# Optimization experiments

Measured on AMD Instinct MI355X. Metric: run time of the kernel, lower is better.

Reference implementation:

```python
import jax, jax.numpy as jnp
import numpy as np

EPS_NORM = 1e-12  # F.normalize eps
EPS_LOG = 1e-10
COMMITMENT_COST = 0.25


def setup_inputs() -> dict:
    key = jax.random.key(0)
    k1, k2 = jax.random.split(key)
    x = jax.random.normal(k1, (32, 256, 32, 32), dtype=jnp.float32)
    # nn.Embedding weight init: uniform(-1, 1)
    W = jax.random.uniform(k2, (1024, 256), dtype=jnp.float32, minval=-1.0, maxval=1.0)
    return {"x": x, "W": W, "n": 2}


def reference(x, W, n):
    sg = jax.lax.stop_gradient
    # NCHW -> NHWC
    inputs = jnp.transpose(x, (0, 2, 3, 1))
    B, H, Wd, D = inputs.shape
    K = W.shape[0]
    flat = inputs.reshape(-1, D)                       # [N, D]
    N = flat.shape[0]
    # squared euclidean distances via matmul: [N, K]
    distances = (jnp.sum(flat * flat, axis=1, keepdims=True)
                 + jnp.sum(W * W, axis=1)
                 - 2.0 * jnp.matmul(flat, W.T))
    # topk of -distances -> n smallest distances
    neg_vals, encoding_indices = jax.lax.top_k(-distances, n)  # [N, n]
    inv_dist = 1.0 / (-neg_vals)                        # 1/distance, [N, n]
    norm = jnp.maximum(jnp.sqrt(jnp.sum(inv_dist * inv_dist, axis=-1, keepdims=True)), EPS_NORM)
    weights = sg(inv_dist / norm)                       # detached in torch
    # scatter weights into one-hot-ish encodings [N, K]
    rows = jnp.arange(N)[:, None]
    encodings = jnp.zeros((N, K), dtype=flat.dtype).at[rows, encoding_indices].set(weights)
    quantized = jnp.matmul(encodings, W).reshape(B, H, Wd, D)
    e_latent_loss = jnp.mean((sg(quantized) - inputs) ** 2)
    q_latent_loss = jnp.mean((quantized - sg(inputs)) ** 2)
    loss = q_latent_loss + COMMITMENT_COST * e_latent_loss
    # straight-through
    quantized_st = inputs + sg(quantized - inputs)
    avg_probs = jnp.mean(encodings, axis=0)
    perplexity = jnp.exp(-jnp.sum(avg_probs * jnp.log(avg_probs + EPS_LOG)))
    return loss, jnp.transpose(quantized_st, (0, 3, 1, 2)), perplexity, encodings
```

## Files before the change

kernel.cpp:

```cpp
#include <hip/hip_runtime.h>
#include <math.h>

#define NROWS 32768
#define DIMS  256
#define KCODES 1024

typedef __attribute__((ext_vector_type(8))) short short8;
typedef __attribute__((ext_vector_type(4))) float f32x4;

static const size_t OFF_WB     = 8388608;
static const size_t OFF_WNORM  = OFF_WB + 131072;
static const size_t OFF_ENCSUM = OFF_WNORM + 1024;
static const size_t OFF_LOSSP  = OFF_ENCSUM + 1024;
static const size_t OFF_WND    = OFF_LOSSP + 8192;

static const size_t OUT_Q    = 1;
static const size_t OUT_PERP = 8388609;
static const size_t OUT_ENC  = 8388610;

__device__ inline unsigned short f2bf(float f) {
    unsigned int u = __float_as_uint(f);
    unsigned int r = u + 0x7FFFu + ((u >> 16) & 1u);
    return (unsigned short)(r >> 16);
}

__device__ inline float packdi(float d, int code) {
    return __uint_as_float((__float_as_uint(d) & 0xFFFFFC00u) | (unsigned)code);
}

__device__ __forceinline__ void gl_lds16(const void* gsrc, void* ldst) {
    typedef const __attribute__((address_space(1))) unsigned int GU;
    typedef __attribute__((address_space(3))) unsigned int LU;
    __builtin_amdgcn_global_load_lds((GU*)gsrc, (LU*)ldst, 16, 0, 0);
}

__global__ __launch_bounds__(256) void wprep(const float* __restrict__ Wm,
                                             unsigned short* __restrict__ Wb,
                                             float* __restrict__ wnorm,
                                             double* __restrict__ wnormd,
                                             float* __restrict__ enc_sum)
{
    const int r = blockIdx.x * 4 + (threadIdx.x >> 6);
    const int lane = threadIdx.x & 63;
    float4 v = ((const float4*)(Wm + (size_t)r * 256))[lane];
    ushort4 o;
    o.x = f2bf(v.x); o.y = f2bf(v.y); o.z = f2bf(v.z); o.w = f2bf(v.w);
    const int d0 = lane * 4;
    const int kk = d0 >> 5, quad = (d0 >> 3) & 3, jb = d0 & 7;
    const int tt = r >> 4, col = r & 15;
    const size_t idx = (size_t)tt * 4096 + (size_t)((kk * 4 + quad) * 16 + col) * 8 + jb;
    *(ushort4*)(Wb + idx) = o;
    double s = (double)v.x*(double)v.x + (double)v.y*(double)v.y
             + (double)v.z*(double)v.z + (double)v.w*(double)v.w;
    #pragma unroll
    for (int off = 32; off > 0; off >>= 1) s += __shfl_down(s, off);
    if (lane == 0) { wnormd[r] = s; wnorm[r] = (float)s; }
    if (blockIdx.x == 0) {
        #pragma unroll
        for (int q = 0; q < 4; ++q) enc_sum[threadIdx.x * 4 + q] = 0.0f;
    }
}

__global__ __launch_bounds__(512, 4) void gemm_topk_quant(
    const float* __restrict__ x, const unsigned short* __restrict__ Wb,
    const float* __restrict__ wnorm, const double* __restrict__ wnd,
    const float* __restrict__ Wm,
    float* __restrict__ enc_sum,
    float* __restrict__ enc,
    float* __restrict__ outq, float* __restrict__ loss_part)
{
    __shared__ __align__(16) char lds[65536];
    float*  sCd   = (float*)lds;
    float*  qtile = (float*)lds;
    double* rd    = (double*)(lds + 34816);
    double* rnr   = (double*)(lds + 38912);
    int*    s0    = (int*)(lds + 39424);
    int*    s1    = (int*)(lds + 39680);
    float*  sw0   = (float*)(lds + 39936);
    float*  sw1   = (float*)(lds + 40192);
    double* sredd = (double*)(lds + 40448);
    int*    mIdx  = (int*)(lds + 40960);
    unsigned short* xtile = (unsigned short*)(lds + 32768);

    const int t    = threadIdx.x;
    const int wave = t >> 6;
    const int g    = wave & 3;
    const int h    = wave >> 2;
    const int lane = t & 63;
    const int col  = lane & 15;
    const int quad = lane >> 4;
    const int r0   = blockIdx.x * 64;
    const int b    = r0 >> 10;
    const int hw0  = r0 & 1023;
    const float* xblk = x + (size_t)b * 262144 + hw0;

    const int row = t >> 3;
    const int q8  = t & 7;

    const char* wb_bytes = (const char*)Wb;
    const size_t src_wave = (size_t)h * 262144 + (size_t)g * 4096;
    const int    lds_wave = h * 16384 + g * 4096;
    {
        const char* src = wb_bytes + src_wave;
        char* dstl = lds + lds_wave;
        #pragma unroll
        for (int q = 0; q < 4; ++q)
            gl_lds16(src + q * 1024 + lane * 16, dstl + q * 1024);
    }

    float xs[32];
    {
        const float* xr = xblk + row;
        #pragma unroll
        for (int p2 = 0; p2 < 2; ++p2)
            #pragma unroll
            for (int j = 0; j < 16; ++j)
                xs[p2 * 16 + j] = xr[(size_t)(p2 * 128 + q8 * 16 + j) * 1024];
    }

    #pragma unroll
    for (int p2 = 0; p2 < 2; ++p2)
        #pragma unroll
        for (int j4 = 0; j4 < 4; ++j4) {
            ushort4 o;
            o.x = f2bf(xs[p2 * 16 + j4 * 4 + 0]);
            o.y = f2bf(xs[p2 * 16 + j4 * 4 + 1]);
            o.z = f2bf(xs[p2 * 16 + j4 * 4 + 2]);
            o.w = f2bf(xs[p2 * 16 + j4 * 4 + 3]);
            const int xi = (row * 256 + p2 * 128 + q8 * 16 + j4 * 4) ^ ((row & 7) << 3);
            *(ushort4*)(xtile + xi) = o;
        }
    __syncthreads();

    short8 af[8];
    #pragma unroll
    for (int kk = 0; kk < 8; ++kk) {
        const int xi = ((g * 16 + col) * 256 + kk * 32 + quad * 8) ^ ((col & 7) << 3);
        af[kk] = *(const short8*)(xtile + xi);
    }
    __syncthreads();

    float m0[4], m1[4], m2[4];
    #pragma unroll
    for (int r = 0; r < 4; ++r) { m0[r] = 3.4e38f; m1[r] = 3.4e38f; m2[r] = 3.4e38f; }

    for (int cc = 0; cc < 16; ++cc) {
        if (cc < 15) {
            const char* src = wb_bytes + src_wave + (size_t)(cc + 1) * 16384;
            char* dstl = lds + ((cc + 1) & 1) * 32768 + lds_wave;
            #pragma unroll
            for (int q = 0; q < 4; ++q)
                gl_lds16(src + q * 1024 + lane * 16, dstl + q * 1024);
        }
        const char* bb = lds + (cc & 1) * 32768 + h * 16384;
        f32x4 acc0 = {0.f, 0.f, 0.f, 0.f};
        f32x4 acc1 = {0.f, 0.f, 0.f, 0.f};
        #pragma unroll
        for (int kk = 0; kk < 8; ++kk) {
            short8 b0 = *(const short8*)(bb + kk * 1024 + lane * 16);
            short8 b1 = *(const short8*)(bb + 8192 + kk * 1024 + lane * 16);
            acc0 = __builtin_amdgcn_mfma_f32_16x16x32_bf16(af[kk], b0, acc0, 0, 0, 0);
            acc1 = __builtin_amdgcn_mfma_f32_16x16x32_bf16(af[kk], b1, acc1, 0, 0, 0);
        }
        const int code0 = h * 512 + cc * 32 + col;
        const int code1 = code0 + 16;
        const float wn0 = wnorm[code0];
        const float wn1 = wnorm[code1];
        #pragma unroll
        for (int r = 0; r < 4; ++r) {
            float pv0 = packdi(fmaf(-2.0f, acc0[r], wn0), code0);
            float t0  = fmaxf(m0[r], pv0); m0[r] = fminf(m0[r], pv0);
            float t1  = fmaxf(m1[r], t0);  m1[r] = fminf(m1[r], t0);
            m2[r] = fminf(m2[r], t1);
            float pv1 = packdi(fmaf(-2.0f, acc1[r], wn1), code1);
            t0 = fmaxf(m0[r], pv1); m0[r] = fminf(m0[r], pv1);
            t1 = fmaxf(m1[r], t0);  m1[r] = fminf(m1[r], t0);
            m2[r] = fminf(m2[r], t1);
        }
        __syncthreads();
    }

    #pragma unroll
    for (int r = 0; r < 4; ++r) {
        const int rl = g * 16 + quad * 4 + r;
        const int s  = h * 48 + col * 3;
        sCd[(s + 0) * 66 + rl] = m0[r];
        sCd[(s + 1) * 66 + rl] = m1[r];
        sCd[(s + 2) * 66 + rl] = m2[r];
    }
    __syncthreads();

    {
        float a0 = 3.4e38f, a1 = 3.4e38f, a2 = 3.4e38f, a3 = 3.4e38f,
              a4 = 3.4e38f, a5 = 3.4e38f, a6 = 3.4e38f, a7 = 3.4e38f;
        #pragma unroll
        for (int i = 0; i < 12; ++i) {
            float d = sCd[(q8 * 12 + i) * 66 + row];
            if (d < a7) {
                a7 = d; float tf;
                if (a7 < a6) { tf = a7; a7 = a6; a6 = tf; }
                if (a6 < a5) { tf = a6; a6 = a5; a5 = tf; }
                if (a5 < a4) { tf = a5; a5 = a4; a4 = tf; }
                if (a4 < a3) { tf = a4; a4 = a3; a3 = tf; }
                if (a3 < a2) { tf = a3; a3 = a2; a2 = tf; }
                if (a2 < a1) { tf = a2; a2 = a1; a1 = tf; }
                if (a1 < a0) { tf = a1; a1 = a0; a0 = tf; }
            }
        }
        float sel = 3.4e38f;
        #pragma unroll
        for (int q = 0; q < 8; ++q) {
            float m = a0;
            m = fminf(m, __shfl_xor(m, 1));
            m = fminf(m, __shfl_xor(m, 2));
            m = fminf(m, __shfl_xor(m, 4));
            if (q8 == q) sel = m;
            if (a0 == m) { a0 = a1; a1 = a2; a2 = a3; a3 = a4;
                           a4 = a5; a5 = a6; a6 = a7; a7 = 3.4e38f; }
        }
        mIdx[row * 8 + q8] = (int)(__float_as_uint(sel) & 1023u);
    }
    __syncthreads();

    {
        int cd[8];
        #pragma unroll
        for (int c8 = 0; c8 < 8; ++c8) cd[c8] = mIdx[row * 8 + c8];
        double dot[8];
        #pragma unroll
        for (int c8 = 0; c8 < 8; ++c8) dot[c8] = 0.0;
        double rn = 0.0;
        #pragma unroll
        for (int v = 0; v < 8; ++v) {
            const int d0 = (v >> 2) * 128 + q8 * 16 + (v & 3) * 4;
            const double x0 = (double)xs[v * 4 + 0];
            const double x1 = (double)xs[v * 4 + 1];
            const double x2 = (double)xs[v * 4 + 2];
            const double x3 = (double)xs[v * 4 + 3];
            rn += x0*x0 + x1*x1 + x2*x2 + x3*x3;
            #pragma unroll
            for (int c8 = 0; c8 < 8; ++c8) {
                const float4 wv = *(const float4*)(Wm + (size_t)cd[c8] * 256 + d0);
                dot[c8] += x0 * (double)wv.x + x1 * (double)wv.y
                         + x2 * (double)wv.z + x3 * (double)wv.w;
            }
        }
        #pragma unroll
        for (int m = 1; m < 8; m <<= 1) {
            #pragma unroll
            for (int c8 = 0; c8 < 8; ++c8) dot[c8] += __shfl_xor(dot[c8], m);
            rn += __shfl_xor(rn, m);
        }
        int myc = 0; double mydot = 0.0;
        #pragma unroll
        for (int c8 = 0; c8 < 8; ++c8)
            if (q8 == c8) { myc = cd[c8]; mydot = dot[c8]; }
        rd[row * 8 + q8] = wnd[myc] - 2.0 * mydot;
        if (q8 == 0) rnr[row] = rn;
    }
    __syncthreads();

    if (t < 64) {
        double rn = rnr[t];
        double d0 = 1e300, d1 = 1e300; int b0 = 1 << 30, b1 = 1 << 30;
        #pragma unroll
        for (int q = 0; q < 8; ++q) {
            double d = rd[t * 8 + q];
            int    c = mIdx[t * 8 + q];
            if (d < d0 || (d == d0 && c < b0)) { d1 = d0; b1 = b0; d0 = d; b0 = c; }
            else if (d < d1 || (d == d1 && c < b1)) { d1 = d; b1 = c; }
        }
        double D0 = rn + d0;
        double D1 = rn + d1;
        double inv0 = 1.0 / D0, inv1 = 1.0 / D1;
        double nrm = sqrt(inv0 * inv0 + inv1 * inv1);
        if (nrm < 1e-12) nrm = 1e-12;
        float w0 = (float)(inv0 / nrm);
        float w1 = (float)(inv1 / nrm);
        s0[t] = b0; s1[t] = b1; sw0[t] = w0; sw1[t] = w1;
        atomicAdd(&enc_sum[b0], w0);
        atomicAdd(&enc_sum[b1], w1);
    }
    __syncthreads();

    #pragma unroll
    for (int rr = 0; rr < 8; ++rr) {
        const int rw = wave * 8 + rr;
        const int i0 = s0[rw], i1 = s1[rw];
        const float w0 = sw0[rw], w1 = sw1[rw];
        f32x4* dst = (f32x4*)(enc + (size_t)(r0 + rw) * KCODES);
        #pragma unroll
        for (int it = 0; it < 4; ++it) {
            const int base = it * 256 + lane * 4;
            f32x4 v;
            v.x = (base + 0 == i0) ? w0 : ((base + 0 == i1) ? w1 : 0.0f);
            v.y = (base + 1 == i0) ? w0 : ((base + 1 == i1) ? w1 : 0.0f);
            v.z = (base + 2 == i0) ? w0 : ((base + 2 == i1) ? w1 : 0.0f);
            v.w = (base + 3 == i0) ? w0 : ((base + 3 == i1) ? w1 : 0.0f);
            dst[it * 64 + lane] = v;
        }
    }

    double ls = 0.0;
    #pragma unroll
    for (int p2 = 0; p2 < 2; ++p2) {
        const int   cA = s0[row], cB = s1[row];
        const float w0 = sw0[row], w1 = sw1[row];
        const float* W0 = Wm + (size_t)cA * 256 + p2 * 128 + q8 * 16;
        const float* W1 = Wm + (size_t)cB * 256 + p2 * 128 + q8 * 16;
        #pragma unroll
        for (int v4 = 0; v4 < 4; ++v4) {
            const float4 a  = *(const float4*)(W0 + v4 * 4);
            const float4 bv = *(const float4*)(W1 + v4 * 4);
            float q0 = w0 * a.x + w1 * bv.x;
            float q1 = w0 * a.y + w1 * bv.y;
            float q2 = w0 * a.z + w1 * bv.z;
            float q3 = w0 * a.w + w1 * bv.w;
            float e0 = q0 - xs[p2 * 16 + v4 * 4 + 0];
            float e1 = q1 - xs[p2 * 16 + v4 * 4 + 1];
            float e2 = q2 - xs[p2 * 16 + v4 * 4 + 2];
            float e3 = q3 - xs[p2 * 16 + v4 * 4 + 3];
            ls += (double)(e0*e0 + e1*e1 + e2*e2 + e3*e3);
            const int dl = q8 * 16 + v4 * 4;
            qtile[(dl + 0) * 67 + row] = q0;
            qtile[(dl + 1) * 67 + row] = q1;
            qtile[(dl + 2) * 67 + row] = q2;
            qtile[(dl + 3) * 67 + row] = q3;
        }
        __syncthreads();
        #pragma unroll
        for (int p = 0; p < 4; ++p) {
            const int task = p * 512 + t;
            const int cl   = task >> 4;
            const int hwq  = task & 15;
            f32x4 v;
            v.x = qtile[cl * 67 + hwq * 4 + 0];
            v.y = qtile[cl * 67 + hwq * 4 + 1];
            v.z = qtile[cl * 67 + hwq * 4 + 2];
            v.w = qtile[cl * 67 + hwq * 4 + 3];
            *(f32x4*)(outq + ((size_t)(b * 256 + p2 * 128 + cl)) * 1024 + hw0 + hwq * 4) = v;
        }
        __syncthreads();
    }

    #pragma unroll
    for (int off = 32; off > 0; off >>= 1) ls += __shfl_down(ls, off);
    if (lane == 0) sredd[wave] = ls;
    __syncthreads();
    if (t == 0) {
        double s = 0.0;
        #pragma unroll
        for (int w = 0; w < 8; ++w) s += sredd[w];
        loss_part[blockIdx.x] = (float)s;
    }
}

__global__ __launch_bounds__(256) void finalize_k(const float* __restrict__ enc_sum,
                                                  const float* __restrict__ loss_part,
                                                  float* __restrict__ out)
{
    __shared__ double sh[256];
    const int t = threadIdx.x;
    double ls = 0.0;
    for (int i = t; i < 512; i += 256) ls += (double)loss_part[i];
    sh[t] = ls; __syncthreads();
    for (int s = 128; s > 0; s >>= 1) { if (t < s) sh[t] += sh[t + s]; __syncthreads(); }
    double loss_sum = sh[0];
    __syncthreads();
    double ps = 0.0;
    for (int k = t; k < KCODES; k += 256) {
        double p = (double)enc_sum[k] / (double)NROWS;
        ps += p * log(p + 1e-10);
    }
    sh[t] = ps; __syncthreads();
    for (int s = 128; s > 0; s >>= 1) { if (t < s) sh[t] += sh[t + s]; __syncthreads(); }
    if (t == 0) {
        out[0]        = (float)(1.25 * loss_sum / 8388608.0);
        out[OUT_PERP] = (float)exp(-sh[0]);
    }
}

extern "C" void kernel_launch(void* const* d_in, const int* in_sizes, int n_in,
                              void* d_out, int out_size, void* d_ws, size_t ws_size,
                              hipStream_t stream)
{
    const float* x  = (const float*)d_in[0];
    const float* Wm = (const float*)d_in[1];
    float* out = (float*)d_out;
    float* ws  = (float*)d_ws;

    unsigned short* Wb      = (unsigned short*)(ws + OFF_WB);
    float*          wnorm   = ws + OFF_WNORM;
    float*          enc_sum = ws + OFF_ENCSUM;
    float*          loss_p  = ws + OFF_LOSSP;
    double*         wnd     = (double*)(ws + OFF_WND);

    wprep<<<KCODES / 4, 256, 0, stream>>>(Wm, Wb, wnorm, wnd, enc_sum);
    gemm_topk_quant<<<NROWS / 64, 512, 0, stream>>>(x, Wb, wnorm, wnd, Wm, enc_sum,
                                                    out + OUT_ENC, out + OUT_Q, loss_p);
    finalize_k<<<1, 256, 0, stream>>>(enc_sum, loss_p, out);
}
```

Before: 263.2 us.

## Halve row tile to 32 rows per block with 256 threads and smaller LDS

```diff
diff --git a/kernel.cpp b/kernel.cpp
--- a/kernel.cpp
+++ b/kernel.cpp
@@ -61,7 +61,7 @@
     }
 }
 
-__global__ __launch_bounds__(512, 4) void gemm_topk_quant(
+__global__ __launch_bounds__(256, 4) void gemm_topk_quant(
     const float* __restrict__ x, const unsigned short* __restrict__ Wb,
     const float* __restrict__ wnorm, const double* __restrict__ wnd,
     const float* __restrict__ Wm,
@@ -69,27 +69,27 @@
     float* __restrict__ enc,
     float* __restrict__ outq, float* __restrict__ loss_part)
 {
-    __shared__ __align__(16) char lds[65536];
+    __shared__ __align__(16) char lds[32768];
     float*  sCd   = (float*)lds;
+    int*    mIdx  = (int*)(lds + 13312);
+    double* rd    = (double*)(lds + 14336);
     float*  qtile = (float*)lds;
-    double* rd    = (double*)(lds + 34816);
-    double* rnr   = (double*)(lds + 38912);
-    int*    s0    = (int*)(lds + 39424);
-    int*    s1    = (int*)(lds + 39680);
-    float*  sw0   = (float*)(lds + 39936);
-    float*  sw1   = (float*)(lds + 40192);
-    double* sredd = (double*)(lds + 40448);
-    int*    mIdx  = (int*)(lds + 40960);
-    unsigned short* xtile = (unsigned short*)(lds + 32768);
+    double* rnr   = (double*)(lds + 16896);
+    int*    s0    = (int*)(lds + 17152);
+    int*    s1    = (int*)(lds + 17280);
+    float*  sw0   = (float*)(lds + 17408);
+    float*  sw1   = (float*)(lds + 17536);
+    double* sredd = (double*)(lds + 17664);
+    unsigned short* xtile = (unsigned short*)(lds + 16384);
 
     const int t    = threadIdx.x;
     const int wave = t >> 6;
-    const int g    = wave & 3;
-    const int h    = wave >> 2;
+    const int g    = wave & 1;
+    const int h    = wave >> 1;
     const int lane = t & 63;
     const int col  = lane & 15;
     const int quad = lane >> 4;
-    const int r0   = blockIdx.x * 64;
+    const int r0   = blockIdx.x * 32;
     const int b    = r0 >> 10;
     const int hw0  = r0 & 1023;
     const float* xblk = x + (size_t)b * 262144 + hw0;
@@ -98,11 +98,9 @@
     const int q8  = t & 7;
 
     const char* wb_bytes = (const char*)Wb;
-    const size_t src_wave = (size_t)h * 262144 + (size_t)g * 4096;
-    const int    lds_wave = h * 16384 + g * 4096;
     {
-        const char* src = wb_bytes + src_wave;
-        char* dstl = lds + lds_wave;
+        const char* src = wb_bytes + (size_t)(h * 32) * 8192 + g * 4096;
+        char* dstl = lds + h * 8192 + g * 4096;
         #pragma unroll
         for (int q = 0; q < 4; ++q)
             gl_lds16(src + q * 1024 + lane * 16, dstl + q * 1024);
@@ -144,38 +142,29 @@
     #pragma unroll
     for (int r = 0; r < 4; ++r) { m0[r] = 3.4e38f; m1[r] = 3.4e38f; m2[r] = 3.4e38f; }
 
-    for (int cc = 0; cc < 16; ++cc) {
-        if (cc < 15) {
-            const char* src = wb_bytes + src_wave + (size_t)(cc + 1) * 16384;
-            char* dstl = lds + ((cc + 1) & 1) * 32768 + lds_wave;
+    for (int cc = 0; cc < 32; ++cc) {
+        if (cc < 31) {
+            const char* src = wb_bytes + (size_t)(h * 32 + cc + 1) * 8192 + g * 4096;
+            char* dstl = lds + ((cc + 1) & 1) * 16384 + h * 8192 + g * 4096;
             #pragma unroll
             for (int q = 0; q < 4; ++q)
                 gl_lds16(src + q * 1024 + lane * 16, dstl + q * 1024);
         }
-        const char* bb = lds + (cc & 1) * 32768 + h * 16384;
-        f32x4 acc0 = {0.f, 0.f, 0.f, 0.f};
-        f32x4 acc1 = {0.f, 0.f, 0.f, 0.f};
+        const char* bb = lds + (cc & 1) * 16384 + h * 8192;
+        f32x4 acc = {0.f, 0.f, 0.f, 0.f};
         #pragma unroll
         for (int kk = 0; kk < 8; ++kk) {
             short8 b0 = *(const short8*)(bb + kk * 1024 + lane * 16);
-            short8 b1 = *(const short8*)(bb + 8192 + kk * 1024 + lane * 16);
-            acc0 = __builtin_amdgcn_mfma_f32_16x16x32_bf16(af[kk], b0, acc0, 0, 0, 0);
-            acc1 = __builtin_amdgcn_mfma_f32_16x16x32_bf16(af[kk], b1, acc1, 0, 0, 0);
-        }
-        const int code0 = h * 512 + cc * 32 + col;
-        const int code1 = code0 + 16;
+            acc = __builtin_amdgcn_mfma_f32_16x16x32_bf16(af[kk], b0, acc, 0, 0, 0);
+        }
+        const int code0 = h * 512 + cc * 16 + col;
         const float wn0 = wnorm[code0];
-        const float wn1 = wnorm[code1];
         #pragma unroll
         for (int r = 0; r < 4; ++r) {
-            float pv0 = packdi(fmaf(-2.0f, acc0[r], wn0), code0);
+            float pv0 = packdi(fmaf(-2.0f, acc[r], wn0), code0);
             float t0  = fmaxf(m0[r], pv0); m0[r] = fminf(m0[r], pv0);
             float t1  = fmaxf(m1[r], t0);  m1[r] = fminf(m1[r], t0);
             m2[r] = fminf(m2[r], t1);
-            float pv1 = packdi(fmaf(-2.0f, acc1[r], wn1), code1);
-            t0 = fmaxf(m0[r], pv1); m0[r] = fminf(m0[r], pv1);
-            t1 = fmaxf(m1[r], t0);  m1[r] = fminf(m1[r], t0);
-            m2[r] = fminf(m2[r], t1);
         }
         __syncthreads();
     }
@@ -184,9 +173,9 @@
     for (int r = 0; r < 4; ++r) {
         const int rl = g * 16 + quad * 4 + r;
         const int s  = h * 48 + col * 3;
-        sCd[(s + 0) * 66 + rl] = m0[r];
-        sCd[(s + 1) * 66 + rl] = m1[r];
-        sCd[(s + 2) * 66 + rl] = m2[r];
+        sCd[(s + 0) * 34 + rl] = m0[r];
+        sCd[(s + 1) * 34 + rl] = m1[r];
+        sCd[(s + 2) * 34 + rl] = m2[r];
     }
     __syncthreads();
 
@@ -195,7 +184,7 @@
               a4 = 3.4e38f, a5 = 3.4e38f, a6 = 3.4e38f, a7 = 3.4e38f;
         #pragma unroll
         for (int i = 0; i < 12; ++i) {
-            float d = sCd[(q8 * 12 + i) * 66 + row];
+            float d = sCd[(q8 * 12 + i) * 34 + row];
             if (d < a7) {
                 a7 = d; float tf;
                 if (a7 < a6) { tf = a7; a7 = a6; a6 = tf; }
@@ -260,7 +249,7 @@
     }
     __syncthreads();
 
-    if (t < 64) {
+    if (t < 32) {
         double rn = rnr[t];
         double d0 = 1e300, d1 = 1e300; int b0 = 1 << 30, b1 = 1 << 30;
         #pragma unroll
@@ -312,32 +301,30 @@
         for (int v4 = 0; v4 < 4; ++v4) {
             const float4 a  = *(const float4*)(W0 + v4 * 4);
             const float4 bv = *(const float4*)(W1 + v4 * 4);
-            float q0 = w0 * a.x + w1 * bv.x;
-            float q1 = w0 * a.y + w1 * bv.y;
-            float q2 = w0 * a.z + w1 * bv.z;
-            float q3 = w0 * a.w + w1 * bv.w;
-            float e0 = q0 - xs[p2 * 16 + v4 * 4 + 0];
-            float e1 = q1 - xs[p2 * 16 + v4 * 4 + 1];
-            float e2 = q2 - xs[p2 * 16 + v4 * 4 + 2];
-            float e3 = q3 - xs[p2 * 16 + v4 * 4 + 3];
+            f32x4 qv;
+            qv.x = w0 * a.x + w1 * bv.x;
+            qv.y = w0 * a.y + w1 * bv.y;
+            qv.z = w0 * a.z + w1 * bv.z;
+            qv.w = w0 * a.w + w1 * bv.w;
+            float e0 = qv.x - xs[p2 * 16 + v4 * 4 + 0];
+            float e1 = qv.y - xs[p2 * 16 + v4 * 4 + 1];
+            float e2 = qv.z - xs[p2 * 16 + v4 * 4 + 2];
+            float e3 = qv.w - xs[p2 * 16 + v4 * 4 + 3];
             ls += (double)(e0*e0 + e1*e1 + e2*e2 + e3*e3);
             const int dl = q8 * 16 + v4 * 4;
-            qtile[(dl + 0) * 67 + row] = q0;
-            qtile[(dl + 1) * 67 + row] = q1;
-            qtile[(dl + 2) * 67 + row] = q2;
-            qtile[(dl + 3) * 67 + row] = q3;
+            *(f32x4*)(qtile + row * 132 + dl) = qv;
         }
         __syncthreads();
         #pragma unroll
         for (int p = 0; p < 4; ++p) {
-            const int task = p * 512 + t;
-            const int cl   = task >> 4;
-            const int hwq  = task & 15;
+            const int task = p * 256 + t;
+            const int cl   = task >> 3;
+            const int hwq  = task & 7;
             f32x4 v;
-            v.x = qtile[cl * 67 + hwq * 4 + 0];
-            v.y = qtile[cl * 67 + hwq * 4 + 1];
-            v.z = qtile[cl * 67 + hwq * 4 + 2];
-            v.w = qtile[cl * 67 + hwq * 4 + 3];
+            v.x = qtile[(hwq * 4 + 0) * 132 + cl];
+            v.y = qtile[(hwq * 4 + 1) * 132 + cl];
+            v.z = qtile[(hwq * 4 + 2) * 132 + cl];
+            v.w = qtile[(hwq * 4 + 3) * 132 + cl];
             *(f32x4*)(outq + ((size_t)(b * 256 + p2 * 128 + cl)) * 1024 + hw0 + hwq * 4) = v;
         }
         __syncthreads();
@@ -350,7 +337,7 @@
     if (t == 0) {
         double s = 0.0;
         #pragma unroll
-        for (int w = 0; w < 8; ++w) s += sredd[w];
+        for (int w = 0; w < 4; ++w) s += sredd[w];
         loss_part[blockIdx.x] = (float)s;
     }
 }
@@ -362,7 +349,7 @@
     __shared__ double sh[256];
     const int t = threadIdx.x;
     double ls = 0.0;
-    for (int i = t; i < 512; i += 256) ls += (double)loss_part[i];
+    for (int i = t; i < 1024; i += 256) ls += (double)loss_part[i];
     sh[t] = ls; __syncthreads();
     for (int s = 128; s > 0; s >>= 1) { if (t < s) sh[t] += sh[t + s]; __syncthreads(); }
     double loss_sum = sh[0];
@@ -396,7 +383,7 @@
     double*         wnd     = (double*)(ws + OFF_WND);
 
     wprep<<<KCODES / 4, 256, 0, stream>>>(Wm, Wb, wnorm, wnd, enc_sum);
-    gemm_topk_quant<<<NROWS / 64, 512, 0, stream>>>(x, Wb, wnorm, wnd, Wm, enc_sum,
+    gemm_topk_quant<<<NROWS / 32, 256, 0, stream>>>(x, Wb, wnorm, wnd, Wm, enc_sum,
                                                     out + OUT_ENC, out + OUT_Q, loss_p);
     finalize_k<<<1, 256, 0, stream>>>(enc_sum, loss_p, out);
 }
```

Measured after the change: 261.0 us. No clear change (-0.8%).
